# Kernel optimization log

Hardware: AMD Instinct MI355X
Metric: run time of the kernel (lower is better)

Reference implementation:

```python
import jax, jax.numpy as jnp
import numpy as np

B, L, D, H = 4, 1024, 1024, 16
HD = D // H  # head_dim = 64


def setup_inputs() -> dict:
    key = jax.random.key(0)
    k1, k2, k3, k4 = jax.random.split(key, 4)
    x = jax.random.normal(k1, (B, L, D), dtype=jnp.float32)
    # causal mask: positions where mask == 0 are filled with -inf
    mask = jnp.tril(jnp.ones((L, L), dtype=bool))[None, None, :, :]  # [1,1,L,L]
    w_qkv = jax.random.normal(k2, (D, 3 * D), dtype=jnp.float32) * (D ** -0.5)
    w_out = jax.random.normal(k3, (D, D), dtype=jnp.float32) * (D ** -0.5)
    rel_pos_bias = jax.random.normal(k4, (H, L, L), dtype=jnp.float32) * 0.02
    return {"x": x, "mask": mask, "w_qkv": w_qkv, "w_out": w_out,
            "rel_pos_bias": rel_pos_bias}


def reference(x, mask, w_qkv, w_out, rel_pos_bias):
    b, l, d = x.shape
    scale = HD ** -0.5
    qkv = (x @ w_qkv).reshape(b, l, 3, H, HD)          # [B,L,3,H,hd]
    q, k, v = qkv[:, :, 0], qkv[:, :, 1], qkv[:, :, 2]  # each [B,L,H,hd]
    # scores: [B,H,Lq,Lk]
    scores = jnp.einsum('bqhd,bkhd->bhqk', q, k) * scale
    scores = scores + rel_pos_bias[None, :, :l, :l]
    scores = jnp.where(mask, scores, -jnp.inf)
    attn = jax.nn.softmax(scores, axis=-1)  # dropout is identity in eval
    out = jnp.einsum('bhqk,bkhd->bqhd', attn, v).reshape(b, l, d)
    return out @ w_out
```

## Files before the change

### kernel.cpp

```cpp
#include <hip/hip_runtime.h>
#include <hip/hip_bf16.h>
#include <math.h>

#define B_  4
#define L_  1024
#define D_  1024
#define H_  16
#define HD_ 64
#define SCALE 0.125f
#define LOG2E 1.44269504f
#define SCALE_L2E (0.125f * 1.44269504f)
#define NEG_BIG -3.0e38f

typedef __bf16 bf16x8 __attribute__((ext_vector_type(8)));
typedef float  f32x4  __attribute__((ext_vector_type(4)));

__device__ __forceinline__ float b2f(unsigned short u) {
    union { unsigned int i; float f; } x; x.i = ((unsigned)u) << 16; return x.f;
}
__device__ __forceinline__ unsigned short f2b(float f) {
    __hip_bfloat16 h = __float2bfloat16(f);
    return *reinterpret_cast<unsigned short*>(&h);
}
__device__ __forceinline__ void gl_lds16(const void* g, void* l) {
    __builtin_amdgcn_global_load_lds(
        (const __attribute__((address_space(1))) void*)g,
        (__attribute__((address_space(3))) void*)l, 16, 0, 0);
}

__global__ __launch_bounds__(256) void convert_x_kernel(
    const float* __restrict__ x, unsigned short* __restrict__ xb)
{
    int i = (blockIdx.x * 256 + threadIdx.x) * 4;
    float4 v = *(const float4*)&x[i];
    ushort4 o = make_ushort4(f2b(v.x), f2b(v.y), f2b(v.z), f2b(v.w));
    *(ushort4*)&xb[i] = o;
}

__global__ __launch_bounds__(256) void transpose_w_kernel(
    const float* __restrict__ w, unsigned short* __restrict__ wt, int N)
{
    __shared__ float tile[32][33];
    const int n0 = blockIdx.x * 32, k0 = blockIdx.y * 32;
    const int tx = threadIdx.x & 31, ty = threadIdx.x >> 5;
#pragma unroll
    for (int i = 0; i < 4; i++) {
        int kk = ty + i * 8;
        tile[kk][tx] = w[(size_t)(k0 + kk) * N + n0 + tx];
    }
    __syncthreads();
#pragma unroll
    for (int i = 0; i < 4; i++) {
        int nn = ty + i * 8;
        wt[(size_t)(n0 + nn) * 1024 + k0 + tx] = f2b(tile[tx][nn]);
    }
}

__device__ __forceinline__ void gemm_core(
    const unsigned short* __restrict__ A, const unsigned short* __restrict__ Bt,
    unsigned short* As, unsigned short* Bs,
    int m0, int n0, int wave, int lane, int wm, int wn,
    f32x4 acc[4][4])
{
    const int srow = lane >> 2, spos = lane & 3;
    const int sc   = spos ^ ((srow >> 1) & 3);
    const int mlane = lane & 15, chunk = lane >> 4;
    const int foff  = mlane * 32 + (chunk ^ ((mlane >> 1) & 3)) * 8;

    for (int k0 = 0; k0 < 1024; k0 += 32) {
#pragma unroll
        for (int t = 0; t < 2; t++) {
            int rb = wave * 32 + t * 16;
            int r  = rb + srow;
            gl_lds16(&A [(size_t)(m0 + r) * 1024 + k0 + sc * 8], &As[rb * 32]);
            gl_lds16(&Bt[(size_t)(n0 + r) * 1024 + k0 + sc * 8], &Bs[rb * 32]);
        }
        __syncthreads();
        bf16x8 af[4], bfr[4];
#pragma unroll
        for (int i = 0; i < 4; i++) {
            af[i]  = *(const bf16x8*)&As[(wm * 64 + i * 16) * 32 + foff];
            bfr[i] = *(const bf16x8*)&Bs[(wn * 64 + i * 16) * 32 + foff];
        }
#pragma unroll
        for (int i = 0; i < 4; i++)
#pragma unroll
            for (int j = 0; j < 4; j++)
                acc[i][j] = __builtin_amdgcn_mfma_f32_16x16x32_bf16(
                    af[i], bfr[j], acc[i][j], 0, 0, 0);
        __syncthreads();
    }
}

__global__ __launch_bounds__(256) void qkv_gemm_kernel(
    const unsigned short* __restrict__ A, const unsigned short* __restrict__ Bt,
    unsigned short* __restrict__ qb, unsigned short* __restrict__ kb,
    unsigned short* __restrict__ vtb)
{
    __shared__ unsigned short As[128 * 32];
    __shared__ unsigned short Bs[128 * 32];
    const int tid  = threadIdx.x;
    const int wave = tid >> 6, lane = tid & 63;
    const int wm = wave >> 1, wn = wave & 1;
    const int m0 = blockIdx.y * 128, n0 = blockIdx.x * 128;
    f32x4 acc[4][4] = {};
    gemm_core(A, Bt, As, Bs, m0, n0, wave, lane, wm, wn, acc);

#pragma unroll
    for (int i = 0; i < 4; i++) {
        int mbase = m0 + wm * 64 + i * 16 + (lane >> 4) * 4;
        int b = mbase >> 10, l = mbase & 1023;
#pragma unroll
        for (int j = 0; j < 4; j++) {
            int n = n0 + wn * 64 + j * 16 + (lane & 15);
            int s = n >> 10, h = (n >> 6) & 15, hd = n & 63;
            if (s == 2) {
                unsigned short tmp[4];
#pragma unroll
                for (int r = 0; r < 4; r++) tmp[r] = f2b(acc[i][j][r]);
                *(ushort4*)&vtb[((size_t)((b * 16 + h) * 64 + hd)) * 1024 + l] =
                    *(ushort4*)tmp;
            } else {
                unsigned short* dst = (s == 0) ? qb : kb;
#pragma unroll
                for (int r = 0; r < 4; r++)
                    dst[(((size_t)(b * 16 + h) * 1024 + (l + r)) << 6) + hd] =
                        f2b(acc[i][j][r]);
            }
        }
    }
}

__global__ __launch_bounds__(256) void out_gemm_kernel(
    const unsigned short* __restrict__ A, const unsigned short* __restrict__ Bt,
    float* __restrict__ out)
{
    __shared__ unsigned short As[128 * 32];
    __shared__ unsigned short Bs[64 * 32];
    const int tid  = threadIdx.x;
    const int wave = tid >> 6, lane = tid & 63;
    const int srow = lane >> 2, spos = lane & 3;
    const int sc   = spos ^ ((srow >> 1) & 3);
    const int mlane = lane & 15, chunk = lane >> 4;
    const int foff  = mlane * 32 + (chunk ^ ((mlane >> 1) & 3)) * 8;
    const int m0 = blockIdx.y * 128, n0 = blockIdx.x * 64;
    f32x4 acc[2][4] = {};

    for (int k0 = 0; k0 < 1024; k0 += 32) {
#pragma unroll
        for (int t = 0; t < 2; t++) {
            int rb = wave * 32 + t * 16;
            gl_lds16(&A[(size_t)(m0 + rb + srow) * 1024 + k0 + sc * 8], &As[rb * 32]);
        }
        {
            int rb = wave * 16;
            gl_lds16(&Bt[(size_t)(n0 + rb + srow) * 1024 + k0 + sc * 8], &Bs[rb * 32]);
        }
        __syncthreads();
        bf16x8 af[2], bfr[4];
#pragma unroll
        for (int i = 0; i < 2; i++)
            af[i]  = *(const bf16x8*)&As[(wave * 32 + i * 16) * 32 + foff];
#pragma unroll
        for (int j = 0; j < 4; j++)
            bfr[j] = *(const bf16x8*)&Bs[(j * 16) * 32 + foff];
#pragma unroll
        for (int i = 0; i < 2; i++)
#pragma unroll
            for (int j = 0; j < 4; j++)
                acc[i][j] = __builtin_amdgcn_mfma_f32_16x16x32_bf16(
                    af[i], bfr[j], acc[i][j], 0, 0, 0);
        __syncthreads();
    }
#pragma unroll
    for (int i = 0; i < 2; i++) {
        int mbase = m0 + wave * 32 + i * 16 + (lane >> 4) * 4;
#pragma unroll
        for (int j = 0; j < 4; j++) {
            int n = n0 + j * 16 + (lane & 15);
#pragma unroll
            for (int r = 0; r < 4; r++)
                out[(size_t)(mbase + r) * 1024 + n] = acc[i][j][r];
        }
    }
}

__global__ __launch_bounds__(256, 4) void attn_mfma_kernel(
    const unsigned short* __restrict__ qb, const unsigned short* __restrict__ kb,
    const unsigned short* __restrict__ vtb, const float* __restrict__ bias,
    unsigned short* __restrict__ ob)
{
    __shared__ unsigned short Qs[64 * 72];
    __shared__ unsigned short Ks[64 * 72];
    __shared__ unsigned short Vts[64 * 72];
    __shared__ unsigned short Ps[64 * 72];

    const int tid  = threadIdx.x;
    const int wave = tid >> 6, lane = tid & 63;
    const int quad = lane >> 4, l16 = lane & 15;
    const int bh = blockIdx.x, b = bh >> 4, h = bh & 15;
    const int qt = blockIdx.y;
    const int q0 = qt * 64;
    const int srow = tid >> 3, scol = (tid & 7) * 8;
    const size_t qkv_base = (size_t)bh * (1024 * 64);
    const int qg_base = q0 + wave * 16 + quad * 4;

#pragma unroll
    for (int i = 0; i < 2; i++) {
        int r = srow + i * 32;
        *(uint4*)&Qs[r * 72 + scol] =
            *(const uint4*)&qb[qkv_base + (size_t)(q0 + r) * 64 + scol];
    }
    uint4 kpre0 = *(const uint4*)&kb[qkv_base + (size_t)srow * 64 + scol];
    uint4 kpre1 = *(const uint4*)&kb[qkv_base + (size_t)(srow + 32) * 64 + scol];
    uint4 vpre0 = *(const uint4*)&vtb[qkv_base + (size_t)srow * 1024 + scol];
    uint4 vpre1 = *(const uint4*)&vtb[qkv_base + (size_t)(srow + 32) * 1024 + scol];

    float bA[16], bB[16];
    {
        const float* bp0 = &bias[((size_t)h * 1024 + qg_base) * 1024];
#pragma unroll
        for (int nt = 0; nt < 4; nt++)
#pragma unroll
            for (int r = 0; r < 4; r++)
                bA[nt * 4 + r] = bp0[(size_t)r * 1024 + nt * 16 + l16] * LOG2E;
    }

    float l_run[4] = {0.f, 0.f, 0.f, 0.f};
    f32x4 Oacc[4] = {};

    __syncthreads();
    bf16x8 af0 = *(const bf16x8*)&Qs[(wave * 16 + l16) * 72 + quad * 8];
    bf16x8 af1 = *(const bf16x8*)&Qs[(wave * 16 + l16) * 72 + 32 + quad * 8];

    auto attn_tile = [&](int kt, float* bcur, float* bnxt) {
        const int k0 = kt * 64;
        *(uint4*)&Ks [(size_t)srow * 72 + scol]        = kpre0;
        *(uint4*)&Ks [(size_t)(srow + 32) * 72 + scol] = kpre1;
        *(uint4*)&Vts[(size_t)srow * 72 + scol]        = vpre0;
        *(uint4*)&Vts[(size_t)(srow + 32) * 72 + scol] = vpre1;
        __syncthreads();
        if (kt < qt) {
            const int kn = k0 + 64;
            kpre0 = *(const uint4*)&kb[qkv_base + (size_t)(kn + srow) * 64 + scol];
            kpre1 = *(const uint4*)&kb[qkv_base + (size_t)(kn + srow + 32) * 64 + scol];
            vpre0 = *(const uint4*)&vtb[qkv_base + (size_t)srow * 1024 + kn + scol];
            vpre1 = *(const uint4*)&vtb[qkv_base + (size_t)(srow + 32) * 1024 + kn + scol];
            const float* bp = &bias[((size_t)h * 1024 + qg_base) * 1024 + kn];
#pragma unroll
            for (int nt = 0; nt < 4; nt++)
#pragma unroll
                for (int r = 0; r < 4; r++)
                    bnxt[nt * 4 + r] = bp[(size_t)r * 1024 + nt * 16 + l16] * LOG2E;
        }
        f32x4 sacc[4] = {};
#pragma unroll
        for (int nt = 0; nt < 4; nt++) {
            bf16x8 bk0 = *(const bf16x8*)&Ks[(nt * 16 + l16) * 72 + quad * 8];
            bf16x8 bk1 = *(const bf16x8*)&Ks[(nt * 16 + l16) * 72 + 32 + quad * 8];
            sacc[nt] = __builtin_amdgcn_mfma_f32_16x16x32_bf16(af0, bk0, sacc[nt], 0, 0, 0);
            sacc[nt] = __builtin_amdgcn_mfma_f32_16x16x32_bf16(af1, bk1, sacc[nt], 0, 0, 0);
        }
        const bool diag = (kt == qt);
#pragma unroll
        for (int nt = 0; nt < 4; nt++) {
            const int kg = k0 + nt * 16 + l16;
#pragma unroll
            for (int r = 0; r < 4; r++) {
                float v = fmaf(sacc[nt][r], SCALE_L2E, bcur[nt * 4 + r]);
                if (diag && kg > qg_base + r) v = NEG_BIG;
                float p = exp2f(v);
                l_run[r] += p;
                Ps[(wave * 16 + quad * 4 + r) * 72 + nt * 16 + l16] = f2b(p);
            }
        }
        bf16x8 pf0 = *(const bf16x8*)&Ps[(wave * 16 + l16) * 72 + quad * 8];
        bf16x8 pf1 = *(const bf16x8*)&Ps[(wave * 16 + l16) * 72 + 32 + quad * 8];
#pragma unroll
        for (int dt = 0; dt < 4; dt++) {
            bf16x8 vf0 = *(const bf16x8*)&Vts[(dt * 16 + l16) * 72 + quad * 8];
            bf16x8 vf1 = *(const bf16x8*)&Vts[(dt * 16 + l16) * 72 + 32 + quad * 8];
            Oacc[dt] = __builtin_amdgcn_mfma_f32_16x16x32_bf16(pf0, vf0, Oacc[dt], 0, 0, 0);
            Oacc[dt] = __builtin_amdgcn_mfma_f32_16x16x32_bf16(pf1, vf1, Oacc[dt], 0, 0, 0);
        }
        __syncthreads();
    };

    for (int kt = 0; kt <= qt; kt += 2) {
        attn_tile(kt, bA, bB);
        if (kt + 1 <= qt) attn_tile(kt + 1, bB, bA);
    }

#pragma unroll
    for (int r = 0; r < 4; r++) {
        float s = l_run[r];
        s += __shfl_xor(s, 1);
        s += __shfl_xor(s, 2);
        s += __shfl_xor(s, 4);
        s += __shfl_xor(s, 8);
        float inv = 1.0f / s;
        int qg = q0 + wave * 16 + quad * 4 + r;
#pragma unroll
        for (int dt = 0; dt < 4; dt++)
            ob[((size_t)(b * 1024 + qg)) * 1024 + h * 64 + dt * 16 + l16] =
                f2b(Oacc[dt][r] * inv);
    }
}


extern "C" void kernel_launch(void* const* d_in, const int* in_sizes, int n_in,
                              void* d_out, int out_size, void* d_ws, size_t ws_size,
                              hipStream_t stream) {
    const float* x     = (const float*)d_in[0];
    const float* w_qkv = (const float*)d_in[2];
    const float* w_out = (const float*)d_in[3];
    const float* bias  = (const float*)d_in[4];
    float* out = (float*)d_out;

    char* ws = (char*)d_ws;
    unsigned short* xb     = (unsigned short*)ws;              ws += (size_t)4096 * 1024 * 2;
    unsigned short* wqkvT  = (unsigned short*)ws;              ws += (size_t)3072 * 1024 * 2;
    unsigned short* woutT  = (unsigned short*)ws;              ws += (size_t)1024 * 1024 * 2;
    unsigned short* qb     = (unsigned short*)ws;              ws += (size_t)4096 * 1024 * 2;
    unsigned short* kb     = (unsigned short*)ws;              ws += (size_t)4096 * 1024 * 2;
    unsigned short* vtb    = (unsigned short*)ws;              ws += (size_t)4096 * 1024 * 2;
    unsigned short* ab     = (unsigned short*)ws;

    convert_x_kernel<<<4096, 256, 0, stream>>>(x, xb);
    transpose_w_kernel<<<dim3(96, 32), 256, 0, stream>>>(w_qkv, wqkvT, 3072);
    transpose_w_kernel<<<dim3(32, 32), 256, 0, stream>>>(w_out, woutT, 1024);

    qkv_gemm_kernel<<<dim3(24, 32), 256, 0, stream>>>(xb, wqkvT, qb, kb, vtb);
    attn_mfma_kernel<<<dim3(64, 16), 256, 0, stream>>>(qb, kb, vtb, bias, ab);
    out_gemm_kernel<<<dim3(16, 32), 256, 0, stream>>>(ab, woutT, out);
}
```

Measured before the change: 223.3 us.

## Pair causal query tiles per block and load K/V fragments directly from global

Each attention block now handles two query tiles (qt and 15-qt), which balances the triangular causal work across blocks and halves the grid. K and V^T fragments are read straight from global memory into registers per wave instead of being staged through shared memory, so the block-wide barriers go away. Only a small per-wave P buffer stays in LDS. The cost is redundant global/L2 reads of K/V by each of the four waves, higher register pressure (launch bounds dropped to 2), and no software prefetch of K/V.

New measurement: 251.1 us. 1.12x slower.

```diff
diff --git a/kernel.cpp b/kernel.cpp
--- a/kernel.cpp
+++ b/kernel.cpp
@@ -185,125 +185,119 @@
     }
 }
 
-__global__ __launch_bounds__(256, 4) void attn_mfma_kernel(
+__global__ __launch_bounds__(256, 2) void attn_mfma_kernel(
     const unsigned short* __restrict__ qb, const unsigned short* __restrict__ kb,
     const unsigned short* __restrict__ vtb, const float* __restrict__ bias,
     unsigned short* __restrict__ ob)
 {
-    __shared__ unsigned short Qs[64 * 72];
-    __shared__ unsigned short Ks[64 * 72];
-    __shared__ unsigned short Vts[64 * 72];
-    __shared__ unsigned short Ps[64 * 72];
+    __shared__ unsigned short Ps[4 * 16 * 72];
 
     const int tid  = threadIdx.x;
     const int wave = tid >> 6, lane = tid & 63;
     const int quad = lane >> 4, l16 = lane & 15;
     const int bh = blockIdx.x, b = bh >> 4, h = bh & 15;
-    const int qt = blockIdx.y;
-    const int q0 = qt * 64;
-    const int srow = tid >> 3, scol = (tid & 7) * 8;
-    const size_t qkv_base = (size_t)bh * (1024 * 64);
-    const int qg_base = q0 + wave * 16 + quad * 4;
-
-#pragma unroll
-    for (int i = 0; i < 2; i++) {
-        int r = srow + i * 32;
-        *(uint4*)&Qs[r * 72 + scol] =
-            *(const uint4*)&qb[qkv_base + (size_t)(q0 + r) * 64 + scol];
-    }
-    uint4 kpre0 = *(const uint4*)&kb[qkv_base + (size_t)srow * 64 + scol];
-    uint4 kpre1 = *(const uint4*)&kb[qkv_base + (size_t)(srow + 32) * 64 + scol];
-    uint4 vpre0 = *(const uint4*)&vtb[qkv_base + (size_t)srow * 1024 + scol];
-    uint4 vpre1 = *(const uint4*)&vtb[qkv_base + (size_t)(srow + 32) * 1024 + scol];
-
-    float bA[16], bB[16];
-    {
-        const float* bp0 = &bias[((size_t)h * 1024 + qg_base) * 1024];
+    const size_t base = (size_t)bh * (1024 * 64);
+    unsigned short* myPs = &Ps[wave * 16 * 72];
+
+    for (int half = 0; half < 2; half++) {
+        const int qt = half ? (15 - (int)blockIdx.y) : (int)blockIdx.y;
+        const int q0 = qt * 64;
+        const int qrow = q0 + wave * 16;
+        const int qg_base = qrow + quad * 4;
+
+        const unsigned short* qp = &qb[base + (size_t)(qrow + l16) * 64 + quad * 8];
+        bf16x8 af0 = *(const bf16x8*)qp;
+        bf16x8 af1 = *(const bf16x8*)(qp + 32);
+
+        float l_run[4] = {0.f, 0.f, 0.f, 0.f};
+        f32x4 Oacc[4] = {};
+
+        float bA[16], bB[16];
+        const float* bp_base = &bias[((size_t)h * 1024 + qg_base) * 1024];
 #pragma unroll
         for (int nt = 0; nt < 4; nt++)
 #pragma unroll
             for (int r = 0; r < 4; r++)
-                bA[nt * 4 + r] = bp0[(size_t)r * 1024 + nt * 16 + l16] * LOG2E;
-    }
-
-    float l_run[4] = {0.f, 0.f, 0.f, 0.f};
-    f32x4 Oacc[4] = {};
-
-    __syncthreads();
-    bf16x8 af0 = *(const bf16x8*)&Qs[(wave * 16 + l16) * 72 + quad * 8];
-    bf16x8 af1 = *(const bf16x8*)&Qs[(wave * 16 + l16) * 72 + 32 + quad * 8];
-
-    auto attn_tile = [&](int kt, float* bcur, float* bnxt) {
-        const int k0 = kt * 64;
-        *(uint4*)&Ks [(size_t)srow * 72 + scol]        = kpre0;
-        *(uint4*)&Ks [(size_t)(srow + 32) * 72 + scol] = kpre1;
-        *(uint4*)&Vts[(size_t)srow * 72 + scol]        = vpre0;
-        *(uint4*)&Vts[(size_t)(srow + 32) * 72 + scol] = vpre1;
-        __syncthreads();
-        if (kt < qt) {
-            const int kn = k0 + 64;
-            kpre0 = *(const uint4*)&kb[qkv_base + (size_t)(kn + srow) * 64 + scol];
-            kpre1 = *(const uint4*)&kb[qkv_base + (size_t)(kn + srow + 32) * 64 + scol];
-            vpre0 = *(const uint4*)&vtb[qkv_base + (size_t)srow * 1024 + kn + scol];
-            vpre1 = *(const uint4*)&vtb[qkv_base + (size_t)(srow + 32) * 1024 + kn + scol];
-            const float* bp = &bias[((size_t)h * 1024 + qg_base) * 1024 + kn];
-#pragma unroll
-            for (int nt = 0; nt < 4; nt++)
-#pragma unroll
-                for (int r = 0; r < 4; r++)
-                    bnxt[nt * 4 + r] = bp[(size_t)r * 1024 + nt * 16 + l16] * LOG2E;
-        }
-        f32x4 sacc[4] = {};
-#pragma unroll
-        for (int nt = 0; nt < 4; nt++) {
-            bf16x8 bk0 = *(const bf16x8*)&Ks[(nt * 16 + l16) * 72 + quad * 8];
-            bf16x8 bk1 = *(const bf16x8*)&Ks[(nt * 16 + l16) * 72 + 32 + quad * 8];
-            sacc[nt] = __builtin_amdgcn_mfma_f32_16x16x32_bf16(af0, bk0, sacc[nt], 0, 0, 0);
-            sacc[nt] = __builtin_amdgcn_mfma_f32_16x16x32_bf16(af1, bk1, sacc[nt], 0, 0, 0);
-        }
-        const bool diag = (kt == qt);
-#pragma unroll
-        for (int nt = 0; nt < 4; nt++) {
-            const int kg = k0 + nt * 16 + l16;
-#pragma unroll
-            for (int r = 0; r < 4; r++) {
-                float v = fmaf(sacc[nt][r], SCALE_L2E, bcur[nt * 4 + r]);
-                if (diag && kg > qg_base + r) v = NEG_BIG;
-                float p = exp2f(v);
-                l_run[r] += p;
-                Ps[(wave * 16 + quad * 4 + r) * 72 + nt * 16 + l16] = f2b(p);
-            }
-        }
-        bf16x8 pf0 = *(const bf16x8*)&Ps[(wave * 16 + l16) * 72 + quad * 8];
-        bf16x8 pf1 = *(const bf16x8*)&Ps[(wave * 16 + l16) * 72 + 32 + quad * 8];
-#pragma unroll
-        for (int dt = 0; dt < 4; dt++) {
-            bf16x8 vf0 = *(const bf16x8*)&Vts[(dt * 16 + l16) * 72 + quad * 8];
-            bf16x8 vf1 = *(const bf16x8*)&Vts[(dt * 16 + l16) * 72 + 32 + quad * 8];
-            Oacc[dt] = __builtin_amdgcn_mfma_f32_16x16x32_bf16(pf0, vf0, Oacc[dt], 0, 0, 0);
-            Oacc[dt] = __builtin_amdgcn_mfma_f32_16x16x32_bf16(pf1, vf1, Oacc[dt], 0, 0, 0);
-        }
-        __syncthreads();
-    };
-
-    for (int kt = 0; kt <= qt; kt += 2) {
-        attn_tile(kt, bA, bB);
-        if (kt + 1 <= qt) attn_tile(kt + 1, bB, bA);
-    }
-
-#pragma unroll
-    for (int r = 0; r < 4; r++) {
-        float s = l_run[r];
-        s += __shfl_xor(s, 1);
-        s += __shfl_xor(s, 2);
-        s += __shfl_xor(s, 4);
-        s += __shfl_xor(s, 8);
-        float inv = 1.0f / s;
-        int qg = q0 + wave * 16 + quad * 4 + r;
-#pragma unroll
-        for (int dt = 0; dt < 4; dt++)
-            ob[((size_t)(b * 1024 + qg)) * 1024 + h * 64 + dt * 16 + l16] =
-                f2b(Oacc[dt][r] * inv);
+                bA[nt * 4 + r] = bp_base[(size_t)r * 1024 + nt * 16 + l16] * LOG2E;
+
+        auto attn_tile = [&](int kt, float* bcur, float* bnxt) {
+            const int k0 = kt * 64;
+            bf16x8 bk[8];
+#pragma unroll
+            for (int nt = 0; nt < 4; nt++) {
+                const unsigned short* kp =
+                    &kb[base + (size_t)(k0 + nt * 16 + l16) * 64 + quad * 8];
+                bk[nt * 2 + 0] = *(const bf16x8*)kp;
+                bk[nt * 2 + 1] = *(const bf16x8*)(kp + 32);
+            }
+            bf16x8 vf[8];
+#pragma unroll
+            for (int dt = 0; dt < 4; dt++) {
+                const unsigned short* vp =
+                    &vtb[base + (size_t)(dt * 16 + l16) * 1024 + k0 + quad * 8];
+                vf[dt * 2 + 0] = *(const bf16x8*)vp;
+                vf[dt * 2 + 1] = *(const bf16x8*)(vp + 32);
+            }
+            if (kt < qt) {
+                const float* bp = bp_base + (kt + 1) * 64;
+#pragma unroll
+                for (int nt = 0; nt < 4; nt++)
+#pragma unroll
+                    for (int r = 0; r < 4; r++)
+                        bnxt[nt * 4 + r] =
+                            bp[(size_t)r * 1024 + nt * 16 + l16] * LOG2E;
+            }
+            f32x4 sacc[4] = {};
+#pragma unroll
+            for (int nt = 0; nt < 4; nt++) {
+                sacc[nt] = __builtin_amdgcn_mfma_f32_16x16x32_bf16(
+                    af0, bk[nt * 2 + 0], sacc[nt], 0, 0, 0);
+                sacc[nt] = __builtin_amdgcn_mfma_f32_16x16x32_bf16(
+                    af1, bk[nt * 2 + 1], sacc[nt], 0, 0, 0);
+            }
+            const bool diag = (kt == qt);
+#pragma unroll
+            for (int nt = 0; nt < 4; nt++) {
+                const int kg = k0 + nt * 16 + l16;
+#pragma unroll
+                for (int r = 0; r < 4; r++) {
+                    float v = fmaf(sacc[nt][r], SCALE_L2E, bcur[nt * 4 + r]);
+                    if (diag && kg > qg_base + r) v = NEG_BIG;
+                    float p = exp2f(v);
+                    l_run[r] += p;
+                    myPs[(quad * 4 + r) * 72 + nt * 16 + l16] = f2b(p);
+                }
+            }
+            bf16x8 pf0 = *(const bf16x8*)&myPs[l16 * 72 + quad * 8];
+            bf16x8 pf1 = *(const bf16x8*)&myPs[l16 * 72 + 32 + quad * 8];
+#pragma unroll
+            for (int dt = 0; dt < 4; dt++) {
+                Oacc[dt] = __builtin_amdgcn_mfma_f32_16x16x32_bf16(
+                    pf0, vf[dt * 2 + 0], Oacc[dt], 0, 0, 0);
+                Oacc[dt] = __builtin_amdgcn_mfma_f32_16x16x32_bf16(
+                    pf1, vf[dt * 2 + 1], Oacc[dt], 0, 0, 0);
+            }
+        };
+
+        for (int kt = 0; kt <= qt; kt += 2) {
+            attn_tile(kt, bA, bB);
+            if (kt + 1 <= qt) attn_tile(kt + 1, bB, bA);
+        }
+
+#pragma unroll
+        for (int r = 0; r < 4; r++) {
+            float s = l_run[r];
+            s += __shfl_xor(s, 1);
+            s += __shfl_xor(s, 2);
+            s += __shfl_xor(s, 4);
+            s += __shfl_xor(s, 8);
+            float inv = 1.0f / s;
+            int qg = qg_base + r;
+#pragma unroll
+            for (int dt = 0; dt < 4; dt++)
+                ob[((size_t)(b * 1024 + qg)) * 1024 + h * 64 + dt * 16 + l16] =
+                    f2b(Oacc[dt][r] * inv);
+        }
     }
 }
 
@@ -331,6 +325,6 @@
     transpose_w_kernel<<<dim3(32, 32), 256, 0, stream>>>(w_out, woutT, 1024);
 
     qkv_gemm_kernel<<<dim3(24, 32), 256, 0, stream>>>(xb, wqkvT, qb, kb, vtb);
-    attn_mfma_kernel<<<dim3(64, 16), 256, 0, stream>>>(qb, kb, vtb, bias, ab);
+    attn_mfma_kernel<<<dim3(64, 8), 256, 0, stream>>>(qb, kb, vtb, bias, ab);
     out_gemm_kernel<<<dim3(16, 32), 256, 0, stream>>>(ab, woutT, out);
 }
```

## Merge prep kernels and transpose MFMA operands for vectorized epilogue stores

Applied to the files above, without the earlier changes.

Folds the x conversion and both weight transposes into a single prep kernel, removing two launches. Swaps the A/B operands of the MFMA in both GEMMs so each lane holds four consecutive N values, letting the Q/K and output epilogues use vector stores (ushort4 / float4) instead of scalar ones, while the V^T store becomes scalar. The attention kernel now references a qg_base variable that may be defined in the unseen portion.

New measurement: 222.4 us. Within noise of the previous version (-0.4%).

```diff
diff --git a/kernel.cpp b/kernel.cpp
--- a/kernel.cpp
+++ b/kernel.cpp
@@ -28,20 +28,30 @@
         (__attribute__((address_space(3))) void*)l, 16, 0, 0);
 }
 
-__global__ __launch_bounds__(256) void convert_x_kernel(
-    const float* __restrict__ x, unsigned short* __restrict__ xb)
-{
-    int i = (blockIdx.x * 256 + threadIdx.x) * 4;
-    float4 v = *(const float4*)&x[i];
-    ushort4 o = make_ushort4(f2b(v.x), f2b(v.y), f2b(v.z), f2b(v.w));
-    *(ushort4*)&xb[i] = o;
-}
-
-__global__ __launch_bounds__(256) void transpose_w_kernel(
-    const float* __restrict__ w, unsigned short* __restrict__ wt, int N)
-{
+__global__ __launch_bounds__(256) void prep_kernel(
+    const float* __restrict__ x, const float* __restrict__ w_qkv,
+    const float* __restrict__ w_out, unsigned short* __restrict__ xb,
+    unsigned short* __restrict__ wqkvT, unsigned short* __restrict__ woutT)
+{
+    const int bid = blockIdx.x;
+    if (bid < 4096) {
+        int i = (bid * 256 + threadIdx.x) * 4;
+        float4 v = *(const float4*)&x[i];
+        ushort4 o = make_ushort4(f2b(v.x), f2b(v.y), f2b(v.z), f2b(v.w));
+        *(ushort4*)&xb[i] = o;
+        return;
+    }
     __shared__ float tile[32][33];
-    const int n0 = blockIdx.x * 32, k0 = blockIdx.y * 32;
+    const float* w; unsigned short* wt; int N, n0, k0;
+    if (bid < 7168) {
+        int b2 = bid - 4096;
+        w = w_qkv; wt = wqkvT; N = 3072;
+        n0 = (b2 % 96) * 32; k0 = (b2 / 96) * 32;
+    } else {
+        int b3 = bid - 7168;
+        w = w_out; wt = woutT; N = 1024;
+        n0 = (b3 % 32) * 32; k0 = (b3 / 32) * 32;
+    }
     const int tx = threadIdx.x & 31, ty = threadIdx.x >> 5;
 #pragma unroll
     for (int i = 0; i < 4; i++) {
@@ -87,7 +97,7 @@
 #pragma unroll
             for (int j = 0; j < 4; j++)
                 acc[i][j] = __builtin_amdgcn_mfma_f32_16x16x32_bf16(
-                    af[i], bfr[j], acc[i][j], 0, 0, 0);
+                    bfr[i], af[j], acc[i][j], 0, 0, 0);
         __syncthreads();
     }
 }
@@ -101,31 +111,33 @@
     __shared__ unsigned short Bs[128 * 32];
     const int tid  = threadIdx.x;
     const int wave = tid >> 6, lane = tid & 63;
+    const int quad = lane >> 4, l16 = lane & 15;
     const int wm = wave >> 1, wn = wave & 1;
     const int m0 = blockIdx.y * 128, n0 = blockIdx.x * 128;
     f32x4 acc[4][4] = {};
     gemm_core(A, Bt, As, Bs, m0, n0, wave, lane, wm, wn, acc);
 
+    const int s = n0 >> 10;
 #pragma unroll
     for (int i = 0; i < 4; i++) {
-        int mbase = m0 + wm * 64 + i * 16 + (lane >> 4) * 4;
-        int b = mbase >> 10, l = mbase & 1023;
+        int n_base = n0 + wn * 64 + i * 16 + quad * 4;
+        int h = (n_base >> 6) & 15, hd0 = n_base & 63;
 #pragma unroll
         for (int j = 0; j < 4; j++) {
-            int n = n0 + wn * 64 + j * 16 + (lane & 15);
-            int s = n >> 10, h = (n >> 6) & 15, hd = n & 63;
+            int m = m0 + wm * 64 + j * 16 + l16;
+            int b = m >> 10, l = m & 1023;
             if (s == 2) {
-                unsigned short tmp[4];
-#pragma unroll
-                for (int r = 0; r < 4; r++) tmp[r] = f2b(acc[i][j][r]);
-                *(ushort4*)&vtb[((size_t)((b * 16 + h) * 64 + hd)) * 1024 + l] =
-                    *(ushort4*)tmp;
+#pragma unroll
+                for (int r = 0; r < 4; r++)
+                    vtb[((size_t)((b * 16 + h) * 64 + hd0 + r)) * 1024 + l] =
+                        f2b(acc[i][j][r]);
             } else {
                 unsigned short* dst = (s == 0) ? qb : kb;
-#pragma unroll
-                for (int r = 0; r < 4; r++)
-                    dst[(((size_t)(b * 16 + h) * 1024 + (l + r)) << 6) + hd] =
-                        f2b(acc[i][j][r]);
+                unsigned short tmp[4];
+#pragma unroll
+                for (int r = 0; r < 4; r++) tmp[r] = f2b(acc[i][j][r]);
+                *(ushort4*)&dst[(((size_t)(b * 16 + h) * 1024 + l) << 6) + hd0] =
+                    *(ushort4*)tmp;
             }
         }
     }
@@ -139,12 +151,13 @@
     __shared__ unsigned short Bs[64 * 32];
     const int tid  = threadIdx.x;
     const int wave = tid >> 6, lane = tid & 63;
+    const int quad = lane >> 4, l16 = lane & 15;
     const int srow = lane >> 2, spos = lane & 3;
     const int sc   = spos ^ ((srow >> 1) & 3);
     const int mlane = lane & 15, chunk = lane >> 4;
     const int foff  = mlane * 32 + (chunk ^ ((mlane >> 1) & 3)) * 8;
     const int m0 = blockIdx.y * 128, n0 = blockIdx.x * 64;
-    f32x4 acc[2][4] = {};
+    f32x4 acc[4][2] = {};
 
     for (int k0 = 0; k0 < 1024; k0 += 32) {
 #pragma unroll
@@ -165,22 +178,22 @@
         for (int j = 0; j < 4; j++)
             bfr[j] = *(const bf16x8*)&Bs[(j * 16) * 32 + foff];
 #pragma unroll
-        for (int i = 0; i < 2; i++)
-#pragma unroll
-            for (int j = 0; j < 4; j++)
-                acc[i][j] = __builtin_amdgcn_mfma_f32_16x16x32_bf16(
-                    af[i], bfr[j], acc[i][j], 0, 0, 0);
-        __syncthreads();
-    }
-#pragma unroll
-    for (int i = 0; i < 2; i++) {
-        int mbase = m0 + wave * 32 + i * 16 + (lane >> 4) * 4;
-#pragma unroll
-        for (int j = 0; j < 4; j++) {
-            int n = n0 + j * 16 + (lane & 15);
-#pragma unroll
-            for (int r = 0; r < 4; r++)
-                out[(size_t)(mbase + r) * 1024 + n] = acc[i][j][r];
+        for (int jn = 0; jn < 4; jn++)
+#pragma unroll
+            for (int im = 0; im < 2; im++)
+                acc[jn][im] = __builtin_amdgcn_mfma_f32_16x16x32_bf16(
+                    bfr[jn], af[im], acc[jn][im], 0, 0, 0);
+        __syncthreads();
+    }
+#pragma unroll
+    for (int jn = 0; jn < 4; jn++) {
+        int n_base = n0 + jn * 16 + quad * 4;
+#pragma unroll
+        for (int im = 0; im < 2; im++) {
+            int m = m0 + wave * 32 + im * 16 + l16;
+            float4 o = make_float4(acc[jn][im][0], acc[jn][im][1],
+                                   acc[jn][im][2], acc[jn][im][3]);
+            *(float4*)&out[(size_t)m * 1024 + n_base] = o;
         }
     }
 }
@@ -299,7 +312,7 @@
         s += __shfl_xor(s, 4);
         s += __shfl_xor(s, 8);
         float inv = 1.0f / s;
-        int qg = q0 + wave * 16 + quad * 4 + r;
+        int qg = qg_base + r;
 #pragma unroll
         for (int dt = 0; dt < 4; dt++)
             ob[((size_t)(b * 1024 + qg)) * 1024 + h * 64 + dt * 16 + l16] =
@@ -326,10 +339,7 @@
     unsigned short* vtb    = (unsigned short*)ws;              ws += (size_t)4096 * 1024 * 2;
     unsigned short* ab     = (unsigned short*)ws;
 
-    convert_x_kernel<<<4096, 256, 0, stream>>>(x, xb);
-    transpose_w_kernel<<<dim3(96, 32), 256, 0, stream>>>(w_qkv, wqkvT, 3072);
-    transpose_w_kernel<<<dim3(32, 32), 256, 0, stream>>>(w_out, woutT, 1024);
-
+    prep_kernel<<<8192, 256, 0, stream>>>(x, w_qkv, w_out, xb, wqkvT, woutT);
     qkv_gemm_kernel<<<dim3(24, 32), 256, 0, stream>>>(xb, wqkvT, qb, kb, vtb);
     attn_mfma_kernel<<<dim3(64, 16), 256, 0, stream>>>(qb, kb, vtb, bias, ab);
     out_gemm_kernel<<<dim3(16, 32), 256, 0, stream>>>(ab, woutT, out);
```
